# Performance work log

Hardware: AMD Instinct MI355X
Metric: run time of the kernel (lower is better)

## Reference

```python
import jax, jax.numpy as jnp
import numpy as np

B, S, T, D, H, DF, E = 16, 1024, 512, 512, 8, 2048, 4
DH = D // H
EPS = 1e-5


def setup_inputs() -> dict:
    key = jax.random.key(0)
    ks = iter(jax.random.split(key, 64))

    def nrm(shape, scale=0.02):
        return jax.random.normal(next(ks), shape, dtype=jnp.float32) * scale

    inp = {
        "x": jax.random.normal(next(ks), (B, S, D), dtype=jnp.float32),
        "cross": jax.random.normal(next(ks), (B, T, D), dtype=jnp.float32),
    }
    for p in ("sa", "ca"):
        for w in ("wq", "wk", "wv", "wo"):
            inp[f"{p}_{w}"] = nrm((D, D))
            inp[f"{p}_b{w[1]}"] = jnp.zeros((D,), jnp.float32)
    inp["gate_w"] = nrm((D, E))
    inp["gate_b"] = jnp.zeros((E,), jnp.float32)
    inp["exp_w1"] = nrm((E, D, DF))
    inp["exp_b1"] = jnp.zeros((E, DF), jnp.float32)
    inp["exp_w2"] = nrm((E, DF, D))
    inp["exp_b2"] = jnp.zeros((E, D), jnp.float32)
    for i in (1, 2, 3):
        inp[f"n{i}_g"] = jnp.ones((D,), jnp.float32)
        inp[f"n{i}_b"] = jnp.zeros((D,), jnp.float32)
    return inp


def layer_norm(x, g, b):
    m = x.mean(-1, keepdims=True)
    v = x.var(-1, keepdims=True)
    return (x - m) * jax.lax.rsqrt(v + EPS) * g + b


def mha(q_in, kv_in, wq, bq, wk, bk, wv, bv, wo, bo, causal):
    Bq, Sq, _ = q_in.shape
    Sk = kv_in.shape[1]
    q = (q_in @ wq + bq).reshape(Bq, Sq, H, DH)
    k = (kv_in @ wk + bk).reshape(Bq, Sk, H, DH)
    v = (kv_in @ wv + bv).reshape(Bq, Sk, H, DH)
    scores = jnp.einsum('bshd,bthd->bhst', q, k) / jnp.sqrt(jnp.float32(DH))
    if causal:
        mask = jnp.tril(jnp.ones((Sq, Sk), dtype=bool))
        scores = jnp.where(mask, scores, jnp.float32(-1e9))
    attn = jax.nn.softmax(scores, axis=-1)
    out = jnp.einsum('bhst,bthd->bshd', attn, v).reshape(Bq, Sq, D)
    return out @ wo + bo


def moe_ffn(x, gw, gb, w1, b1, w2, b2):
    gates = jax.nn.softmax(x @ gw + gb, axis=-1)            # [B,S,E]
    h = jax.nn.relu(jnp.einsum('bsd,edf->bsef', x, w1) + b1)  # [B,S,E,DF]
    yo = jnp.einsum('bsef,efd->bsed', h, w2) + b2            # [B,S,E,D]
    y = jnp.einsum('bse,bsed->bsd', gates, yo)
    imp = gates.mean((0, 1))                                 # importance per expert
    aux = jnp.float32(E) * jnp.sum(imp * imp)                # load-balance penalty
    return y, aux


def reference(x, cross,
              sa_wq, sa_bq, sa_wk, sa_bk, sa_wv, sa_bv, sa_wo, sa_bo,
              ca_wq, ca_bq, ca_wk, ca_bk, ca_wv, ca_bv, ca_wo, ca_bo,
              gate_w, gate_b, exp_w1, exp_b1, exp_w2, exp_b2,
              n1_g, n1_b, n2_g, n2_b, n3_g, n3_b):
    # dropout is identity in eval mode
    x = x + mha(x, x, sa_wq, sa_bq, sa_wk, sa_bk, sa_wv, sa_bv, sa_wo, sa_bo, causal=True)
    x = layer_norm(x, n1_g, n1_b)
    x = x + mha(x, cross, ca_wq, ca_bq, ca_wk, ca_bk, ca_wv, ca_bv, ca_wo, ca_bo, causal=False)
    x = layer_norm(x, n2_g, n2_b)
    y, aux_loss = moe_ffn(x, gate_w, gate_b, exp_w1, exp_b1, exp_w2, exp_b2)
    out = layer_norm(x + y, n3_g, n3_b)
    return out, aux_loss
```

## Files before the change

kernel.cpp:

```cpp
#include <hip/hip_runtime.h>
#include <stdint.h>
#include <stddef.h>

typedef unsigned short bf16u;
typedef __attribute__((ext_vector_type(8))) short short8;
typedef __attribute__((ext_vector_type(4))) float f32x4;

__device__ __forceinline__ bf16u f2bf(float f) {
  union { float f; unsigned u; } v; v.f = f;
  unsigned r = v.u + 0x7FFFu + ((v.u >> 16) & 1u);
  return (bf16u)(r >> 16);
}

#define GL16(g, l) __builtin_amdgcn_global_load_lds( \
    (const __attribute__((address_space(1))) unsigned int*)(g), \
    (__attribute__((address_space(3))) unsigned int*)(l), 16, 0, 0)

enum { EPI_BF16 = 0, EPI_RELU_GATE = 1, EPI_QKV = 2, EPI_RES = 3, EPI_ACC = 4, EPI_KV = 5 };

template<int EPI, int BN>
__global__ __launch_bounds__(512, 2) void gemm256(
    const bf16u* __restrict__ A, const bf16u* __restrict__ BT,
    const float* __restrict__ bias, const float* __restrict__ res,
    const float* __restrict__ gates,
    bf16u* __restrict__ o1, bf16u* __restrict__ o2, bf16u* __restrict__ o3,
    float* __restrict__ of,
    int N, int K, int LDA, int LDB, int slog, int egate, int firste)
{
  constexpr int NI = BN / 64;
  constexpr int NB = BN / 64;
  constexpr int LOADS = 4 + NB;
  __shared__ bf16u Al[2][256 * 64];
  __shared__ bf16u Bl[2][BN * 64];

  const int tid = threadIdx.x, lane = tid & 63, w = tid >> 6;
  const int wm = w >> 2, wn = w & 3;
  const int rl = lane & 15, g4 = lane >> 4, rsub = g4 * 4;

  const int cpx = gridDim.x >> 3;
  const int bid = (blockIdx.x & 7) * cpx + (blockIdx.x >> 3);
  const int nbt = N / BN;
  const int mt = bid / nbt, nt = bid - mt * nbt;
  const int bm = mt * 256, bn = nt * BN;

  const int lrow = lane >> 3;
  const int lcol = ((lane & 7) * 8) ^ (lrow * 8);

  auto stage = [&](int buf, int kt) {
    const int ko = kt * 64 + lcol;
    #pragma unroll
    for (int i = 0; i < 4; ++i) {
      const int r = i * 64 + w * 8;
      GL16(A + (size_t)(bm + r + lrow) * LDA + ko, &Al[buf][r * 64]);
    }
    #pragma unroll
    for (int i = 0; i < NB; ++i) {
      const int r = i * 64 + w * 8;
      GL16(BT + (size_t)(bn + r + lrow) * LDB + ko, &Bl[buf][r * 64]);
    }
  };

  f32x4 acc[8][NI] = {};
  const int NT = K >> 6;

  stage(0, 0);
  stage(1, 1);
  asm volatile("s_waitcnt vmcnt(%0)" :: "n"(LOADS) : "memory");
  __builtin_amdgcn_sched_barrier(0);
  __builtin_amdgcn_s_barrier();
  __builtin_amdgcn_sched_barrier(0);

  int cur = 0;
  for (int kt = 0; kt < NT; ++kt) {
    short8 a0[8], b0[NI];
    #pragma unroll
    for (int mi = 0; mi < 8; ++mi) {
      const int r = wm * 128 + mi * 16 + rl;
      a0[mi] = *(const short8*)&Al[cur][r * 64 + ((g4 * 8) ^ ((r & 7) * 8))];
    }
    #pragma unroll
    for (int ni = 0; ni < NI; ++ni) {
      const int r = wn * (NI * 16) + ni * 16 + rl;
      b0[ni] = *(const short8*)&Bl[cur][r * 64 + ((g4 * 8) ^ ((r & 7) * 8))];
    }
    __builtin_amdgcn_s_setprio(1);
    #pragma unroll
    for (int mi = 0; mi < 8; ++mi)
      #pragma unroll
      for (int ni = 0; ni < NI; ++ni)
        acc[mi][ni] = __builtin_amdgcn_mfma_f32_16x16x32_bf16(a0[mi], b0[ni], acc[mi][ni], 0, 0, 0);
    __builtin_amdgcn_s_setprio(0);

    short8 a1[8], b1[NI];
    #pragma unroll
    for (int mi = 0; mi < 8; ++mi) {
      const int r = wm * 128 + mi * 16 + rl;
      a1[mi] = *(const short8*)&Al[cur][r * 64 + ((32 + g4 * 8) ^ ((r & 7) * 8))];
    }
    #pragma unroll
    for (int ni = 0; ni < NI; ++ni) {
      const int r = wn * (NI * 16) + ni * 16 + rl;
      b1[ni] = *(const short8*)&Bl[cur][r * 64 + ((32 + g4 * 8) ^ ((r & 7) * 8))];
    }
    asm volatile("s_waitcnt lgkmcnt(0)" ::: "memory");
    __builtin_amdgcn_sched_barrier(0);
    __builtin_amdgcn_s_barrier();
    __builtin_amdgcn_sched_barrier(0);

    if (kt + 2 < NT) stage(cur, kt + 2);

    __builtin_amdgcn_s_setprio(1);
    #pragma unroll
    for (int mi = 0; mi < 8; ++mi)
      #pragma unroll
      for (int ni = 0; ni < NI; ++ni)
        acc[mi][ni] = __builtin_amdgcn_mfma_f32_16x16x32_bf16(a1[mi], b1[ni], acc[mi][ni], 0, 0, 0);
    __builtin_amdgcn_s_setprio(0);

    if (kt + 1 < NT) {
      if (kt + 2 < NT) {
        asm volatile("s_waitcnt vmcnt(%0)" :: "n"(LOADS) : "memory");
      } else {
        asm volatile("s_waitcnt vmcnt(0)" ::: "memory");
      }
      __builtin_amdgcn_sched_barrier(0);
      __builtin_amdgcn_s_barrier();
      __builtin_amdgcn_sched_barrier(0);
    }
    cur ^= 1;
  }

  const int r0 = bm + wm * 128, c0 = bn + wn * (NI * 16);
  #pragma unroll
  for (int ni = 0; ni < NI; ++ni) {
    const int col = c0 + ni * 16 + rl;
    const float bs = bias ? bias[col] : 0.f;
    #pragma unroll
    for (int mi = 0; mi < 8; ++mi) {
      const f32x4 v = acc[mi][ni];
      #pragma unroll
      for (int jj = 0; jj < 4; ++jj) {
        const int row = r0 + mi * 16 + rsub + jj;
        const float val = v[jj] + bs;
        if (EPI == EPI_BF16) {
          o1[(size_t)row * N + col] = f2bf(val);
        } else if (EPI == EPI_RELU_GATE) {
          const float g = gates[(size_t)row * 4 + egate];
          o1[(size_t)row * N + col] = f2bf(g * (val > 0.f ? val : 0.f));
        } else if (EPI == EPI_QKV) {
          if (col < 512) o1[(size_t)row * 512 + col] = f2bf(val);
          else if (col < 1024) o2[(size_t)row * 512 + col - 512] = f2bf(val);
          else {
            const int c = col - 1024;
            const int b_ = row >> slog, t_ = row & ((1 << slog) - 1);
            o3[(((size_t)(b_ * 8 + (c >> 6)) << 6) + (size_t)(c & 63)) * ((size_t)1 << slog) + t_] = f2bf(val);
          }
        } else if (EPI == EPI_KV) {
          if (col < 512) o2[(size_t)row * 512 + col] = f2bf(val);
          else {
            const int c = col - 512;
            const int b_ = row >> slog, t_ = row & ((1 << slog) - 1);
            o3[(((size_t)(b_ * 8 + (c >> 6)) << 6) + (size_t)(c & 63)) * ((size_t)1 << slog) + t_] = f2bf(val);
          }
        } else if (EPI == EPI_RES) {
          of[(size_t)row * N + col] = res[(size_t)row * N + col] + val;
        } else {
          const size_t oi = (size_t)row * N + col;
          of[oi] = firste ? val : (of[oi] + val);
        }
      }
    }
  }
}

template<bool CAUSAL>
__global__ __launch_bounds__(256, 4) void attn_k(
    const bf16u* __restrict__ Q, const bf16u* __restrict__ Kg,
    const bf16u* __restrict__ VT, bf16u* __restrict__ O,
    int Sq, int Sk)
{
  __shared__ bf16u Kl[2][64 * 64];
  __shared__ bf16u Vl[2][64 * 64];
  __shared__ bf16u Pl[64 * 64];
  const int nqt = Sq >> 6;
  const int bh = blockIdx.x / nqt, qt = blockIdx.x - bh * nqt;
  const int b = bh >> 3, h = bh & 7;
  const int tid = threadIdx.x, lane = tid & 63, w = tid >> 6;
  const int rl = lane & 15, g4 = lane >> 4;

  const int qrow = qt * 64 + w * 16 + rl;
  const bf16u* qp = Q + (size_t)(b * Sq + qrow) * 512 + h * 64 + g4 * 8;
  const short8 qf0 = *(const short8*)qp;
  const short8 qf1 = *(const short8*)(qp + 32);

  f32x4 oacc[4] = {};
  float ml = -1e30f, ll = 0.f;
  const int KT = CAUSAL ? (qt + 1) : (Sk >> 6);

  const int str = tid >> 2, stc = tid & 3;
  const int sw_st = (str & 7) << 4;
  const bf16u* kq = Kg + (size_t)(b * Sk + str) * 512 + h * 64 + stc * 8;
  const bf16u* vq = VT + (size_t)(bh * 64 + str) * Sk + stc * 8;
  const int lo0 = str * 128 + ((stc * 16) ^ sw_st);
  const int lo1 = str * 128 + ((stc * 16 + 64) ^ sw_st);

  const int qr = w * 16 + rl;
  char* const pbase = (char*)Pl + qr * 128;
  const int swq = (qr & 7) << 4;

  {
    const short8 k0 = *(const short8*)kq;
    const short8 k1 = *(const short8*)(kq + 32);
    const short8 v0 = *(const short8*)vq;
    const short8 v1 = *(const short8*)(vq + 32);
    *(short8*)((char*)Kl[0] + lo0) = k0;
    *(short8*)((char*)Kl[0] + lo1) = k1;
    *(short8*)((char*)Vl[0] + lo0) = v0;
    *(short8*)((char*)Vl[0] + lo1) = v1;
  }
  __syncthreads();

  int cur = 0;
  for (int kt = 0; kt < KT; ++kt) {
    short8 nk0, nk1, nv0, nv1;
    const bool pre = (kt + 1 < KT);
    if (pre) {
      const bf16u* ks = kq + (size_t)(kt + 1) * 64 * 512;
      const bf16u* vs = vq + (kt + 1) * 64;
      nk0 = *(const short8*)ks;
      nk1 = *(const short8*)(ks + 32);
      nv0 = *(const short8*)vs;
      nv1 = *(const short8*)(vs + 32);
    }

    const bf16u* Kc = Kl[cur];
    const bf16u* Vc = Vl[cur];
    f32x4 st[4] = {};
    #pragma unroll
    for (int mi = 0; mi < 4; ++mi) {
      const int kr = mi * 16 + rl;
      const char* kb_ = (const char*)Kc + kr * 128;
      const int sw = (kr & 7) << 4;
      const short8 kf0 = *(const short8*)(kb_ + ((g4 * 16) ^ sw));
      const short8 kf1 = *(const short8*)(kb_ + ((g4 * 16 + 64) ^ sw));
      st[mi] = __builtin_amdgcn_mfma_f32_16x16x32_bf16(kf0, qf0, st[mi], 0, 0, 0);
      st[mi] = __builtin_amdgcn_mfma_f32_16x16x32_bf16(kf1, qf1, st[mi], 0, 0, 0);
    }

    const float SC = 0.125f * 1.44269504f;
    float sv[16];
    float pm = -1e30f;
    if (CAUSAL && kt == qt) {
      const int qg = qt * 64 + qr;
      #pragma unroll
      for (int mi = 0; mi < 4; ++mi)
        #pragma unroll
        for (int jj = 0; jj < 4; ++jj) {
          float s = st[mi][jj] * SC;
          const int kgi = kt * 64 + mi * 16 + g4 * 4 + jj;
          if (kgi > qg) s = -1e30f;
          sv[mi * 4 + jj] = s;
          pm = fmaxf(pm, s);
        }
    } else {
      #pragma unroll
      for (int mi = 0; mi < 4; ++mi)
        #pragma unroll
        for (int jj = 0; jj < 4; ++jj) {
          const float s = st[mi][jj] * SC;
          sv[mi * 4 + jj] = s;
          pm = fmaxf(pm, s);
        }
    }
    pm = fmaxf(pm, __shfl_xor(pm, 16));
    pm = fmaxf(pm, __shfl_xor(pm, 32));
    const float mnew = fmaxf(ml, pm);
    const float alpha = exp2f(ml - mnew);
    float ps = 0.f;
    bf16u pb[16];
    #pragma unroll
    for (int ii = 0; ii < 16; ++ii) {
      const float p = exp2f(sv[ii] - mnew);
      ps += p;
      pb[ii] = f2bf(p);
    }
    ps += __shfl_xor(ps, 16);
    ps += __shfl_xor(ps, 32);
    ll = ll * alpha + ps;
    ml = mnew;

    #pragma unroll
    for (int jj = 0; jj < 4; ++jj) {
      const float aj = __shfl(alpha, g4 * 4 + jj);
      #pragma unroll
      for (int ni = 0; ni < 4; ++ni) oacc[ni][jj] *= aj;
    }

    #pragma unroll
    for (int mi = 0; mi < 4; ++mi) {
      #pragma unroll
      for (int jp = 0; jp < 2; ++jp) {
        const unsigned pk = (unsigned)pb[mi * 4 + jp * 2] | ((unsigned)pb[mi * 4 + jp * 2 + 1] << 16);
        const int kx2 = mi * 32 + g4 * 8 + jp * 4;
        *(unsigned*)(pbase + (kx2 ^ swq)) = pk;
      }
    }
    asm volatile("s_waitcnt lgkmcnt(0)" ::: "memory");
    #pragma unroll
    for (int ks = 0; ks < 2; ++ks) {
      const short8 pf = *(const short8*)(pbase + ((g4 * 16 + ks * 64) ^ swq));
      #pragma unroll
      for (int ni = 0; ni < 4; ++ni) {
        const int vr = ni * 16 + rl;
        const short8 vf = *(const short8*)((const char*)Vc + vr * 128 + ((g4 * 16 + ks * 64) ^ ((vr & 7) << 4)));
        oacc[ni] = __builtin_amdgcn_mfma_f32_16x16x32_bf16(pf, vf, oacc[ni], 0, 0, 0);
      }
    }

    __syncthreads();
    if (pre) {
      const int nb = cur ^ 1;
      *(short8*)((char*)Kl[nb] + lo0) = nk0;
      *(short8*)((char*)Kl[nb] + lo1) = nk1;
      *(short8*)((char*)Vl[nb] + lo0) = nv0;
      *(short8*)((char*)Vl[nb] + lo1) = nv1;
      __syncthreads();
    }
    cur ^= 1;
  }

  #pragma unroll
  for (int jj = 0; jj < 4; ++jj) {
    const float lj = __shfl(ll, g4 * 4 + jj);
    const float inv = 1.f / lj;
    const int row = qt * 64 + w * 16 + g4 * 4 + jj;
    #pragma unroll
    for (int ni = 0; ni < 4; ++ni)
      O[(size_t)(b * Sq + row) * 512 + h * 64 + ni * 16 + rl] = f2bf(oacc[ni][jj] * inv);
  }
}

template<bool ADD, bool BOUT>
__global__ __launch_bounds__(256, 4) void ln_k(
    const float* __restrict__ X, const float* __restrict__ Y,
    const float* __restrict__ gam, const float* __restrict__ bet,
    float* __restrict__ outf, bf16u* __restrict__ outb)
{
  const int row = blockIdx.x * 4 + (threadIdx.x >> 6);
  const int lane = threadIdx.x & 63;
  const float* xp = X + (size_t)row * 512 + lane * 8;
  float v[8];
  {
    const float4 t0 = *(const float4*)xp;
    const float4 t1 = *(const float4*)(xp + 4);
    v[0] = t0.x; v[1] = t0.y; v[2] = t0.z; v[3] = t0.w;
    v[4] = t1.x; v[5] = t1.y; v[6] = t1.z; v[7] = t1.w;
  }
  if (ADD) {
    const float* yp = Y + (size_t)row * 512 + lane * 8;
    const float4 t0 = *(const float4*)yp;
    const float4 t1 = *(const float4*)(yp + 4);
    v[0] += t0.x; v[1] += t0.y; v[2] += t0.z; v[3] += t0.w;
    v[4] += t1.x; v[5] += t1.y; v[6] += t1.z; v[7] += t1.w;
  }
  float s = 0.f, q = 0.f;
  #pragma unroll
  for (int i = 0; i < 8; ++i) { s += v[i]; q += v[i] * v[i]; }
  #pragma unroll
  for (int off = 1; off < 64; off <<= 1) {
    s += __shfl_xor(s, off);
    q += __shfl_xor(q, off);
  }
  const float mean = s * (1.f / 512.f);
  const float var = q * (1.f / 512.f) - mean * mean;
  const float rs = rsqrtf(var + 1e-5f);
  float o[8];
  #pragma unroll
  for (int i = 0; i < 8; ++i) {
    const float g = gam[lane * 8 + i], bb = bet[lane * 8 + i];
    o[i] = (v[i] - mean) * rs * g + bb;
  }
  float* op = outf + (size_t)row * 512 + lane * 8;
  *(float4*)op = make_float4(o[0], o[1], o[2], o[3]);
  *(float4*)(op + 4) = make_float4(o[4], o[5], o[6], o[7]);
  if (BOUT) {
    union { bf16u u[8]; short8 v8; } pk;
    #pragma unroll
    for (int i = 0; i < 8; ++i) pk.u[i] = f2bf(o[i]);
    *(short8*)(outb + (size_t)row * 512 + lane * 8) = pk.v8;
  }
}

__global__ __launch_bounds__(256, 4) void ln_final_k(
    const float* __restrict__ X, const float* __restrict__ Y,
    const float* __restrict__ gates, const float* __restrict__ b2,
    const float* __restrict__ gam, const float* __restrict__ bet,
    float* __restrict__ outf)
{
  const int row = blockIdx.x * 4 + (threadIdx.x >> 6);
  const int lane = threadIdx.x & 63;
  const float4 gv4 = *(const float4*)(gates + (size_t)row * 4);
  float v[8];
  {
    const float* xp = X + (size_t)row * 512 + lane * 8;
    const float* yp = Y + (size_t)row * 512 + lane * 8;
    const float4 t0 = *(const float4*)xp;
    const float4 t1 = *(const float4*)(xp + 4);
    const float4 u0 = *(const float4*)yp;
    const float4 u1 = *(const float4*)(yp + 4);
    v[0] = t0.x + u0.x; v[1] = t0.y + u0.y; v[2] = t0.z + u0.z; v[3] = t0.w + u0.w;
    v[4] = t1.x + u1.x; v[5] = t1.y + u1.y; v[6] = t1.z + u1.z; v[7] = t1.w + u1.w;
  }
  #pragma unroll
  for (int e = 0; e < 4; ++e) {
    const float ge = e == 0 ? gv4.x : e == 1 ? gv4.y : e == 2 ? gv4.z : gv4.w;
    const float4 b0 = *(const float4*)(b2 + e * 512 + lane * 8);
    const float4 b1 = *(const float4*)(b2 + e * 512 + lane * 8 + 4);
    v[0] += ge * b0.x; v[1] += ge * b0.y; v[2] += ge * b0.z; v[3] += ge * b0.w;
    v[4] += ge * b1.x; v[5] += ge * b1.y; v[6] += ge * b1.z; v[7] += ge * b1.w;
  }
  float s = 0.f, q = 0.f;
  #pragma unroll
  for (int i = 0; i < 8; ++i) { s += v[i]; q += v[i] * v[i]; }
  #pragma unroll
  for (int off = 1; off < 64; off <<= 1) {
    s += __shfl_xor(s, off);
    q += __shfl_xor(q, off);
  }
  const float mean = s * (1.f / 512.f);
  const float var = q * (1.f / 512.f) - mean * mean;
  const float rs = rsqrtf(var + 1e-5f);
  float* op = outf + (size_t)row * 512 + lane * 8;
  float o[8];
  #pragma unroll
  for (int i = 0; i < 8; ++i)
    o[i] = (v[i] - mean) * rs * gam[lane * 8 + i] + bet[lane * 8 + i];
  *(float4*)op = make_float4(o[0], o[1], o[2], o[3]);
  *(float4*)(op + 4) = make_float4(o[4], o[5], o[6], o[7]);
}

__global__ __launch_bounds__(256, 4) void gate_k(
    const float* __restrict__ X, const float* __restrict__ gw,
    const float* __restrict__ gb, float* __restrict__ gates,
    float* __restrict__ imp)
{
  __shared__ float sh[4];
  const int tid = threadIdx.x;
  if (tid < 4) sh[tid] = 0.f;
  __syncthreads();
  const int row = blockIdx.x * 4 + (tid >> 6);
  const int lane = tid & 63;
  const float* xr = X + (size_t)row * 512;
  float a0 = 0.f, a1 = 0.f, a2 = 0.f, a3 = 0.f;
  for (int d = lane; d < 512; d += 64) {
    const float xv = xr[d];
    const float4 wv = *(const float4*)(gw + d * 4);
    a0 += xv * wv.x; a1 += xv * wv.y; a2 += xv * wv.z; a3 += xv * wv.w;
  }
  #pragma unroll
  for (int off = 1; off < 64; off <<= 1) {
    a0 += __shfl_xor(a0, off); a1 += __shfl_xor(a1, off);
    a2 += __shfl_xor(a2, off); a3 += __shfl_xor(a3, off);
  }
  if (lane == 0) {
    a0 += gb[0]; a1 += gb[1]; a2 += gb[2]; a3 += gb[3];
    const float m = fmaxf(fmaxf(a0, a1), fmaxf(a2, a3));
    const float e0 = exp2f((a0 - m) * 1.44269504f);
    const float e1 = exp2f((a1 - m) * 1.44269504f);
    const float e2 = exp2f((a2 - m) * 1.44269504f);
    const float e3 = exp2f((a3 - m) * 1.44269504f);
    const float inv = 1.f / (e0 + e1 + e2 + e3);
    float* gr = gates + (size_t)row * 4;
    const float g0 = e0 * inv, g1 = e1 * inv, g2 = e2 * inv, g3 = e3 * inv;
    gr[0] = g0; gr[1] = g1; gr[2] = g2; gr[3] = g3;
    atomicAdd(&sh[0], g0); atomicAdd(&sh[1], g1);
    atomicAdd(&sh[2], g2); atomicAdd(&sh[3], g3);
  }
  __syncthreads();
  if (tid < 4) atomicAdd(&imp[tid], sh[tid]);
}

__global__ void aux_k(const float* __restrict__ imp, float* __restrict__ out) {
  if (threadIdx.x == 0 && blockIdx.x == 0) {
    float s = 0.f;
    #pragma unroll
    for (int e = 0; e < 4; ++e) { const float v = imp[e] * (1.f / 16384.f); s += v * v; }
    out[0] = 4.f * s;
  }
}

__global__ __launch_bounds__(256, 4) void conv_k(const float* __restrict__ in, bf16u* __restrict__ out) {
  const size_t i = ((size_t)blockIdx.x * 256 + threadIdx.x) * 8;
  const float4 a = *(const float4*)(in + i);
  const float4 b = *(const float4*)(in + i + 4);
  union { bf16u u[8]; short8 v; } pk;
  pk.u[0] = f2bf(a.x); pk.u[1] = f2bf(a.y); pk.u[2] = f2bf(a.z); pk.u[3] = f2bf(a.w);
  pk.u[4] = f2bf(b.x); pk.u[5] = f2bf(b.y); pk.u[6] = f2bf(b.z); pk.u[7] = f2bf(b.w);
  *(short8*)(out + i) = pk.v;
}

__global__ __launch_bounds__(256, 4) void trans_k(
    const float* __restrict__ W, bf16u* __restrict__ WT, int K, int N)
{
  __shared__ float t[32][33];
  const int tx = threadIdx.x & 31, ty = threadIdx.x >> 5;
  const int n0 = blockIdx.x * 32, k0 = blockIdx.y * 32;
  #pragma unroll
  for (int i = 0; i < 4; ++i)
    t[ty + i * 8][tx] = W[(size_t)(k0 + ty + i * 8) * N + n0 + tx];
  __syncthreads();
  #pragma unroll
  for (int i = 0; i < 4; ++i)
    WT[(size_t)(n0 + ty + i * 8) * K + k0 + tx] = f2bf(t[tx][ty + i * 8]);
}

extern "C" void kernel_launch(void* const* d_in, const int* in_sizes, int n_in,
                              void* d_out, int out_size, void* d_ws, size_t ws_size,
                              hipStream_t stream)
{
  const int B = 16, S = 1024, T = 512, D = 512, DF = 2048, E = 4;
  const int M = B * S;
  const int Mc = B * T;
  (void)in_sizes; (void)n_in; (void)out_size; (void)ws_size;

  const float* x      = (const float*)d_in[0];
  const float* cross  = (const float*)d_in[1];
  const float* gate_w = (const float*)d_in[18];
  const float* gate_b = (const float*)d_in[19];
  const float* exp_w1 = (const float*)d_in[20];
  const float* exp_b1 = (const float*)d_in[21];
  const float* exp_w2 = (const float*)d_in[22];
  const float* exp_b2 = (const float*)d_in[23];

  char* p = (char*)d_ws;
  auto alloc = [&](size_t bytes) -> char* {
    char* r = p;
    p += (bytes + 255) & ~(size_t)255;
    return r;
  };
  bf16u* xb    = (bf16u*)alloc((size_t)M * D * 2);
  bf16u* crb   = (bf16u*)alloc((size_t)Mc * D * 2);
  bf16u* wT    = (bf16u*)alloc((size_t)8 * D * D * 2);
  bf16u* w1T   = (bf16u*)alloc((size_t)E * DF * D * 2);
  bf16u* w2T   = (bf16u*)alloc((size_t)E * D * DF * 2);
  bf16u* qb    = (bf16u*)alloc((size_t)M * D * 2);
  bf16u* kb    = (bf16u*)alloc((size_t)M * D * 2);
  bf16u* vTb   = (bf16u*)alloc((size_t)M * D * 2);
  bf16u* ao    = (bf16u*)alloc((size_t)M * D * 2);
  float* xf    = (float*)alloc((size_t)M * D * 4);
  bf16u* x2b   = (bf16u*)alloc((size_t)M * D * 2);
  float* gates = (float*)alloc((size_t)M * 4 * 4);
  float* imp   = (float*)alloc(256);
  bf16u* hbuf  = (bf16u*)alloc((size_t)M * DF * 2);
  float* y     = (float*)alloc((size_t)M * D * 4);
  float* qkvb  = (float*)alloc(1536 * 4);
  float* kvb   = (float*)alloc(1024 * 4);

  hipMemsetAsync(imp, 0, 32, stream);
  hipMemcpyAsync(qkvb,        d_in[3], 512 * 4, hipMemcpyDeviceToDevice, stream);
  hipMemcpyAsync(qkvb + 512,  d_in[5], 512 * 4, hipMemcpyDeviceToDevice, stream);
  hipMemcpyAsync(qkvb + 1024, d_in[7], 512 * 4, hipMemcpyDeviceToDevice, stream);
  hipMemcpyAsync(kvb,         d_in[13], 512 * 4, hipMemcpyDeviceToDevice, stream);
  hipMemcpyAsync(kvb + 512,   d_in[15], 512 * 4, hipMemcpyDeviceToDevice, stream);

  conv_k<<<(M * D) / 2048, 256, 0, stream>>>(x, xb);
  conv_k<<<(Mc * D) / 2048, 256, 0, stream>>>(cross, crb);
  for (int i = 0; i < 8; ++i)
    trans_k<<<dim3(D / 32, D / 32), 256, 0, stream>>>((const float*)d_in[2 + 2 * i], wT + (size_t)i * D * D, D, D);
  for (int e = 0; e < E; ++e)
    trans_k<<<dim3(DF / 32, D / 32), 256, 0, stream>>>(exp_w1 + (size_t)e * D * DF, w1T + (size_t)e * DF * D, D, DF);
  for (int e = 0; e < E; ++e)
    trans_k<<<dim3(D / 32, DF / 32), 256, 0, stream>>>(exp_w2 + (size_t)e * DF * D, w2T + (size_t)e * D * DF, DF, D);

  const int gATT = B * 8 * (S / 64);

  gemm256<EPI_QKV, 256><<<(M / 256) * 6, 512, 0, stream>>>(
      xb, wT, qkvb, nullptr, nullptr, qb, kb, vTb, nullptr, 1536, 512, 512, 512, 10, 0, 0);
  attn_k<true><<<gATT, 256, 0, stream>>>(qb, kb, vTb, ao, S, S);
  gemm256<EPI_RES, 128><<<(M / 256) * 4, 512, 0, stream>>>(
      ao, wT + 3 * (size_t)D * D, (const float*)d_in[9], x, nullptr,
      nullptr, nullptr, nullptr, xf, 512, 512, 512, 512, 0, 0, 0);
  ln_k<false, true><<<M / 4, 256, 0, stream>>>(xf, nullptr, (const float*)d_in[24], (const float*)d_in[25], xf, x2b);

  gemm256<EPI_BF16, 128><<<(M / 256) * 4, 512, 0, stream>>>(
      x2b, wT + 4 * (size_t)D * D, (const float*)d_in[11], nullptr, nullptr,
      qb, nullptr, nullptr, nullptr, 512, 512, 512, 512, 0, 0, 0);
  gemm256<EPI_KV, 128><<<(Mc / 256) * 8, 512, 0, stream>>>(
      crb, wT + 5 * (size_t)D * D, kvb, nullptr, nullptr,
      nullptr, kb, vTb, nullptr, 1024, 512, 512, 512, 9, 0, 0);
  attn_k<false><<<gATT, 256, 0, stream>>>(qb, kb, vTb, ao, S, T);
  gemm256<EPI_RES, 128><<<(M / 256) * 4, 512, 0, stream>>>(
      ao, wT + 7 * (size_t)D * D, (const float*)d_in[17], xf, nullptr,
      nullptr, nullptr, nullptr, xf, 512, 512, 512, 512, 0, 0, 0);
  ln_k<false, true><<<M / 4, 256, 0, stream>>>(xf, nullptr, (const float*)d_in[26], (const float*)d_in[27], xf, x2b);

  gate_k<<<M / 4, 256, 0, stream>>>(xf, gate_w, gate_b, gates, imp);
  aux_k<<<1, 64, 0, stream>>>(imp, (float*)d_out + (size_t)M * D);
  for (int e = 0; e < E; ++e) {
    gemm256<EPI_RELU_GATE, 256><<<(M / 256) * 8, 512, 0, stream>>>(
        x2b, w1T + (size_t)e * DF * D, exp_b1 + (size_t)e * DF, nullptr, gates,
        hbuf, nullptr, nullptr, nullptr, 2048, 512, 512, 512, 0, e, 0);
    gemm256<EPI_ACC, 128><<<(M / 256) * 4, 512, 0, stream>>>(
        hbuf, w2T + (size_t)e * D * DF, nullptr, nullptr, nullptr,
        nullptr, nullptr, nullptr, y, 512, 2048, 2048, 2048, 0, 0, e == 0 ? 1 : 0);
  }
  ln_final_k<<<M / 4, 256, 0, stream>>>(xf, y, gates, exp_b2, (const float*)d_in[28], (const float*)d_in[29], (float*)d_out);
}
```

Before: 1.062 ms.

## Replace hand-scheduled two-stage GEMM pipeline with simple double-buffered loop

```diff
diff --git a/kernel.cpp b/kernel.cpp
--- a/kernel.cpp
+++ b/kernel.cpp
@@ -29,7 +29,6 @@
 {
   constexpr int NI = BN / 64;
   constexpr int NB = BN / 64;
-  constexpr int LOADS = 4 + NB;
   __shared__ bf16u Al[2][256 * 64];
   __shared__ bf16u Bl[2][BN * 64];
 
@@ -64,69 +63,33 @@
   const int NT = K >> 6;
 
   stage(0, 0);
-  stage(1, 1);
-  asm volatile("s_waitcnt vmcnt(%0)" :: "n"(LOADS) : "memory");
-  __builtin_amdgcn_sched_barrier(0);
-  __builtin_amdgcn_s_barrier();
-  __builtin_amdgcn_sched_barrier(0);
+  __syncthreads();
 
   int cur = 0;
   for (int kt = 0; kt < NT; ++kt) {
-    short8 a0[8], b0[NI];
-    #pragma unroll
-    for (int mi = 0; mi < 8; ++mi) {
-      const int r = wm * 128 + mi * 16 + rl;
-      a0[mi] = *(const short8*)&Al[cur][r * 64 + ((g4 * 8) ^ ((r & 7) * 8))];
-    }
-    #pragma unroll
-    for (int ni = 0; ni < NI; ++ni) {
-      const int r = wn * (NI * 16) + ni * 16 + rl;
-      b0[ni] = *(const short8*)&Bl[cur][r * 64 + ((g4 * 8) ^ ((r & 7) * 8))];
-    }
-    __builtin_amdgcn_s_setprio(1);
-    #pragma unroll
-    for (int mi = 0; mi < 8; ++mi)
-      #pragma unroll
-      for (int ni = 0; ni < NI; ++ni)
-        acc[mi][ni] = __builtin_amdgcn_mfma_f32_16x16x32_bf16(a0[mi], b0[ni], acc[mi][ni], 0, 0, 0);
-    __builtin_amdgcn_s_setprio(0);
-
-    short8 a1[8], b1[NI];
-    #pragma unroll
-    for (int mi = 0; mi < 8; ++mi) {
-      const int r = wm * 128 + mi * 16 + rl;
-      a1[mi] = *(const short8*)&Al[cur][r * 64 + ((32 + g4 * 8) ^ ((r & 7) * 8))];
-    }
-    #pragma unroll
-    for (int ni = 0; ni < NI; ++ni) {
-      const int r = wn * (NI * 16) + ni * 16 + rl;
-      b1[ni] = *(const short8*)&Bl[cur][r * 64 + ((32 + g4 * 8) ^ ((r & 7) * 8))];
-    }
-    asm volatile("s_waitcnt lgkmcnt(0)" ::: "memory");
-    __builtin_amdgcn_sched_barrier(0);
-    __builtin_amdgcn_s_barrier();
-    __builtin_amdgcn_sched_barrier(0);
-
-    if (kt + 2 < NT) stage(cur, kt + 2);
-
-    __builtin_amdgcn_s_setprio(1);
-    #pragma unroll
-    for (int mi = 0; mi < 8; ++mi)
-      #pragma unroll
-      for (int ni = 0; ni < NI; ++ni)
-        acc[mi][ni] = __builtin_amdgcn_mfma_f32_16x16x32_bf16(a1[mi], b1[ni], acc[mi][ni], 0, 0, 0);
-    __builtin_amdgcn_s_setprio(0);
-
-    if (kt + 1 < NT) {
-      if (kt + 2 < NT) {
-        asm volatile("s_waitcnt vmcnt(%0)" :: "n"(LOADS) : "memory");
-      } else {
-        asm volatile("s_waitcnt vmcnt(0)" ::: "memory");
+    if (kt + 1 < NT) stage(cur ^ 1, kt + 1);
+
+    #pragma unroll
+    for (int kh = 0; kh < 2; ++kh) {
+      short8 av[8], bv[NI];
+      #pragma unroll
+      for (int mi = 0; mi < 8; ++mi) {
+        const int r = wm * 128 + mi * 16 + rl;
+        av[mi] = *(const short8*)&Al[cur][r * 64 + ((kh * 32 + g4 * 8) ^ ((r & 7) * 8))];
       }
-      __builtin_amdgcn_sched_barrier(0);
-      __builtin_amdgcn_s_barrier();
-      __builtin_amdgcn_sched_barrier(0);
-    }
+      #pragma unroll
+      for (int ni = 0; ni < NI; ++ni) {
+        const int r = wn * (NI * 16) + ni * 16 + rl;
+        bv[ni] = *(const short8*)&Bl[cur][r * 64 + ((kh * 32 + g4 * 8) ^ ((r & 7) * 8))];
+      }
+      #pragma unroll
+      for (int mi = 0; mi < 8; ++mi)
+        #pragma unroll
+        for (int ni = 0; ni < NI; ++ni)
+          acc[mi][ni] = __builtin_amdgcn_mfma_f32_16x16x32_bf16(av[mi], bv[ni], acc[mi][ni], 0, 0, 0);
+    }
+
+    __syncthreads();
     cur ^= 1;
   }
 
```

Result: slower. 1.091 ms (+2.7%).
